# Kernel optimization log

Hardware: AMD Instinct MI355X
Metric: run time of the kernel (lower is better)

Reference implementation:

```python
import jax, jax.numpy as jnp
import numpy as np

B, D = 8192, 1024
GATE_BIAS = 0.0
LN_EPS = 1e-5


def _layernorm(x, w, b):
    mu = jnp.mean(x, axis=-1, keepdims=True)
    var = jnp.mean(jnp.square(x - mu), axis=-1, keepdims=True)
    return (x - mu) * jax.lax.rsqrt(var + LN_EPS) * w + b


def setup_inputs() -> dict:
    key = jax.random.key(0)
    ks = jax.random.split(key, 12)
    s_in = 1.0 / np.sqrt(2 * D)  # torch Linear init scale (fan_in = 2*dim)
    return {
        "x": jax.random.normal(ks[0], (B, D), jnp.float32),
        "h": jax.random.normal(ks[1], (B, D), jnp.float32),
        "ln_w": jnp.ones((2 * D,), jnp.float32),
        "ln_b": jnp.zeros((2 * D,), jnp.float32),
        "ln2_w": jnp.ones((2 * D,), jnp.float32),
        "ln2_b": jnp.zeros((2 * D,), jnp.float32),
        "Wg": jax.random.uniform(ks[2], (5 * D, 2 * D), jnp.float32, -s_in, s_in),
        "bg": jax.random.uniform(ks[3], (5 * D,), jnp.float32, -s_in, s_in),
        "Wu": jax.random.uniform(ks[4], (D, 2 * D), jnp.float32, -s_in, s_in),
        "bu": jax.random.uniform(ks[5], (D,), jnp.float32, -s_in, s_in),
    }


def reference(x, h, ln_w, ln_b, ln2_w, ln2_b, Wg, bg, Wu, bu):
    # eval mode: dropout / dropout_mask (ones) / zoneout are identity
    inp = jnp.concatenate([x, h], axis=1)          # [B, 2D]
    inp = _layernorm(inp, ln_w, ln_b)
    gates = inp @ Wg.T + bg                        # [B, 5D]
    g0, g1, g2, g3, g4 = jnp.split(gates, 5, axis=1)
    rx = jax.nn.sigmoid(g0)
    rh = jax.nn.sigmoid(g1)
    z = jax.nn.softmax(jnp.stack([g2, g3, g4 - GATE_BIAS], axis=-1), axis=-1)  # [B, D, 3]
    inp2 = jnp.concatenate([x * rx, h * rh], axis=1)
    inp2 = _layernorm(inp2, ln2_w, ln2_b)
    u = jnp.tanh(inp2 @ Wu.T + bu)                 # [B, D]
    h_new = (jnp.stack([x, h, u], axis=-1) * z).sum(-1)
    return h_new
```

## Files before the change

### kernel.cpp

```cpp
#include <hip/hip_runtime.h>

typedef __attribute__((ext_vector_type(8))) __bf16 bf16x8;
typedef __attribute__((ext_vector_type(4))) float f32x4;

#define B_ROWS 8192
#define D_DIM  1024
#define K_DIM  2048
#define NG     5120

typedef const __attribute__((address_space(1))) void cg_void;
typedef __attribute__((address_space(3))) void lds_void;

__device__ __forceinline__ float bf2f(unsigned short u) {
    union { unsigned int ui; float f; } c; c.ui = ((unsigned int)u) << 16; return c.f;
}
__device__ __forceinline__ unsigned short f2bf(float f) {
    unsigned int u = __float_as_uint(f);
    unsigned int r = u + 0x7fffu + ((u >> 16) & 1u);
    return (unsigned short)(r >> 16);
}
__device__ __forceinline__ float sigm(float v) { return 1.0f / (1.0f + __expf(-v)); }

__global__ __launch_bounds__(256) void cvt2_f32_bf16(const float* __restrict__ wg,
                                                     const float* __restrict__ wu,
                                                     unsigned short* __restrict__ og,
                                                     unsigned short* __restrict__ ou) {
    const int NG4 = 5120 * 2048 / 4;
    const int NU4 = 1024 * 2048 / 4;
    int i = blockIdx.x * 256 + threadIdx.x;
    if (i < NG4) {
        float4 v = reinterpret_cast<const float4*>(wg)[i];
        ushort4 o; o.x = f2bf(v.x); o.y = f2bf(v.y); o.z = f2bf(v.z); o.w = f2bf(v.w);
        reinterpret_cast<ushort4*>(og)[i] = o;
    } else if (i < NG4 + NU4) {
        int j = i - NG4;
        float4 v = reinterpret_cast<const float4*>(wu)[j];
        ushort4 o; o.x = f2bf(v.x); o.y = f2bf(v.y); o.z = f2bf(v.z); o.w = f2bf(v.w);
        reinterpret_cast<ushort4*>(ou)[j] = o;
    }
}

__global__ __launch_bounds__(256) void ln1_kernel(const float* __restrict__ x, const float* __restrict__ h,
                                                  const float* __restrict__ w, const float* __restrict__ b,
                                                  unsigned short* __restrict__ out) {
    const int row = blockIdx.x;
    const int t = threadIdx.x;
    const float4 xv = reinterpret_cast<const float4*>(x + (size_t)row * D_DIM)[t];
    const float4 hv = reinterpret_cast<const float4*>(h + (size_t)row * D_DIM)[t];
    float s  = xv.x + xv.y + xv.z + xv.w + hv.x + hv.y + hv.z + hv.w;
    float s2 = xv.x*xv.x + xv.y*xv.y + xv.z*xv.z + xv.w*xv.w
             + hv.x*hv.x + hv.y*hv.y + hv.z*hv.z + hv.w*hv.w;
#pragma unroll
    for (int off = 32; off > 0; off >>= 1) { s += __shfl_xor(s, off); s2 += __shfl_xor(s2, off); }
    __shared__ float red[8];
    const int wid = t >> 6, lane = t & 63;
    if (lane == 0) { red[wid] = s; red[4 + wid] = s2; }
    __syncthreads();
    s  = red[0] + red[1] + red[2] + red[3];
    s2 = red[4] + red[5] + red[6] + red[7];
    const float mu  = s * (1.0f / K_DIM);
    const float var = s2 * (1.0f / K_DIM) - mu * mu;
    const float inv = rsqrtf(var + 1e-5f);
    const float4 w0 = reinterpret_cast<const float4*>(w)[t];
    const float4 b0 = reinterpret_cast<const float4*>(b)[t];
    const float4 w1 = reinterpret_cast<const float4*>(w + D_DIM)[t];
    const float4 b1 = reinterpret_cast<const float4*>(b + D_DIM)[t];
    ushort4 o0, o1;
    o0.x = f2bf((xv.x - mu) * inv * w0.x + b0.x);
    o0.y = f2bf((xv.y - mu) * inv * w0.y + b0.y);
    o0.z = f2bf((xv.z - mu) * inv * w0.z + b0.z);
    o0.w = f2bf((xv.w - mu) * inv * w0.w + b0.w);
    o1.x = f2bf((hv.x - mu) * inv * w1.x + b1.x);
    o1.y = f2bf((hv.y - mu) * inv * w1.y + b1.y);
    o1.z = f2bf((hv.z - mu) * inv * w1.z + b1.z);
    o1.w = f2bf((hv.w - mu) * inv * w1.w + b1.w);
    reinterpret_cast<ushort4*>(out + (size_t)row * K_DIM)[t] = o0;
    reinterpret_cast<ushort4*>(out + (size_t)row * K_DIM + D_DIM)[t] = o1;
}

__global__ __launch_bounds__(256) void gate_ln2_kernel(const float* __restrict__ x, const float* __restrict__ h,
                                                       const unsigned short* __restrict__ gates,
                                                       const float* __restrict__ w, const float* __restrict__ b,
                                                       unsigned short* __restrict__ out) {
    const int row = blockIdx.x;
    const int t = threadIdx.x;
    const float4 xv = reinterpret_cast<const float4*>(x + (size_t)row * D_DIM)[t];
    const float4 hv = reinterpret_cast<const float4*>(h + (size_t)row * D_DIM)[t];
    const ushort4 g0v = reinterpret_cast<const ushort4*>(gates + (size_t)row * NG)[t];
    const ushort4 g1v = reinterpret_cast<const ushort4*>(gates + (size_t)row * NG + D_DIM)[t];
    float a0 = xv.x * sigm(bf2f(g0v.x));
    float a1 = xv.y * sigm(bf2f(g0v.y));
    float a2 = xv.z * sigm(bf2f(g0v.z));
    float a3 = xv.w * sigm(bf2f(g0v.w));
    float c0 = hv.x * sigm(bf2f(g1v.x));
    float c1 = hv.y * sigm(bf2f(g1v.y));
    float c2 = hv.z * sigm(bf2f(g1v.z));
    float c3 = hv.w * sigm(bf2f(g1v.w));
    float s  = a0 + a1 + a2 + a3 + c0 + c1 + c2 + c3;
    float s2 = a0*a0 + a1*a1 + a2*a2 + a3*a3 + c0*c0 + c1*c1 + c2*c2 + c3*c3;
#pragma unroll
    for (int off = 32; off > 0; off >>= 1) { s += __shfl_xor(s, off); s2 += __shfl_xor(s2, off); }
    __shared__ float red[8];
    const int wid = t >> 6, lane = t & 63;
    if (lane == 0) { red[wid] = s; red[4 + wid] = s2; }
    __syncthreads();
    s  = red[0] + red[1] + red[2] + red[3];
    s2 = red[4] + red[5] + red[6] + red[7];
    const float mu  = s * (1.0f / K_DIM);
    const float var = s2 * (1.0f / K_DIM) - mu * mu;
    const float inv = rsqrtf(var + 1e-5f);
    const float4 w0 = reinterpret_cast<const float4*>(w)[t];
    const float4 b0 = reinterpret_cast<const float4*>(b)[t];
    const float4 w1 = reinterpret_cast<const float4*>(w + D_DIM)[t];
    const float4 b1 = reinterpret_cast<const float4*>(b + D_DIM)[t];
    ushort4 o0, o1;
    o0.x = f2bf((a0 - mu) * inv * w0.x + b0.x);
    o0.y = f2bf((a1 - mu) * inv * w0.y + b0.y);
    o0.z = f2bf((a2 - mu) * inv * w0.z + b0.z);
    o0.w = f2bf((a3 - mu) * inv * w0.w + b0.w);
    o1.x = f2bf((c0 - mu) * inv * w1.x + b1.x);
    o1.y = f2bf((c1 - mu) * inv * w1.y + b1.y);
    o1.z = f2bf((c2 - mu) * inv * w1.z + b1.z);
    o1.w = f2bf((c3 - mu) * inv * w1.w + b1.w);
    reinterpret_cast<ushort4*>(out + (size_t)row * K_DIM)[t] = o0;
    reinterpret_cast<ushort4*>(out + (size_t)row * K_DIM + D_DIM)[t] = o1;
}

#define PH(BUF, H, KQ, LOADB, STAGE_CODE, VMCNT_CODE) do {                                            \
    bf16x8 aF[4];                                                                                     \
    _Pragma("unroll")                                                                                 \
    for (int m = 0; m < 4; ++m)                                                                       \
        aF[m] = *reinterpret_cast<const bf16x8*>(                                                     \
            &smem[((BUF) * 2 + (H)) * 8192 + ((aRdS[m] ^ ((KQ) * 64)) >> 1)]);                        \
    if (LOADB) {                                                                                      \
        _Pragma("unroll")                                                                             \
        for (int n = 0; n < 4; ++n)                                                                   \
            bF[KQ][n] = *reinterpret_cast<const bf16x8*>(                                             \
                &smem[32768 + ((BUF) * 2 + bHalf) * 8192 + ((bRdS[n] ^ ((KQ) * 64)) >> 1)]);          \
    }                                                                                                 \
    STAGE_CODE;                                                                                       \
    VMCNT_CODE;                                                                                       \
    asm volatile("" ::: "memory");                                                                    \
    __builtin_amdgcn_s_barrier();                                                                     \
    asm volatile("" ::: "memory");                                                                    \
    __builtin_amdgcn_s_setprio(1);                                                                    \
    _Pragma("unroll")                                                                                 \
    for (int m = 0; m < 4; ++m)                                                                       \
        _Pragma("unroll")                                                                             \
        for (int n = 0; n < 4; ++n)                                                                   \
            acc[(H) * 4 + m][n] =                                                                     \
                __builtin_amdgcn_mfma_f32_16x16x32_bf16(aF[m], bF[KQ][n], acc[(H) * 4 + m][n], 0, 0, 0);\
    __builtin_amdgcn_s_setprio(0);                                                                    \
    asm volatile("" ::: "memory");                                                                    \
    __builtin_amdgcn_s_barrier();                                                                     \
    asm volatile("" ::: "memory");                                                                    \
} while (0)

#define VMC4 asm volatile("s_waitcnt vmcnt(4)" ::: "memory")
#define VMC0 asm volatile("s_waitcnt vmcnt(0)" ::: "memory")
#define NOVM (void)0

__global__ __launch_bounds__(512, 2) void gemm_gates8(const unsigned short* __restrict__ A,
                                                      const unsigned short* __restrict__ W,
                                                      const float* __restrict__ bias,
                                                      unsigned short* __restrict__ C) {
    constexpr int K = K_DIM;
    constexpr int NT = K / 64;
    constexpr int NI = NT / 2;
    extern __shared__ unsigned short smem[];

    const int tid = threadIdx.x;
    const int bid = blockIdx.x;
    const int lane = tid & 63;
    const int wid = tid >> 6;
    const int wr = wid >> 2;
    const int wc = wid & 3;
    const int fr = lane & 15;
    const int kb = lane >> 4;
    const int bHalf = wc >> 1;
    const int swzl = (fr & 7) << 4;

    int aRdS[4], bRdS[4];
#pragma unroll
    for (int m = 0; m < 4; ++m)
        aRdS[m] = (((wr * 64 + m * 16 + fr) * 128) + kb * 16) ^ swzl;
#pragma unroll
    for (int n = 0; n < 4; ++n)
        bRdS[n] = ((((wc & 1) * 64 + n * 16 + fr) * 128) + kb * 16) ^ swzl;

    int srcRow[2], srcCol[2], ldsDst[2];
#pragma unroll
    for (int l = 0; l < 2; ++l) {
        const int off = (l * 512 + tid) * 16;
        const int r = off >> 7;
        const int offS = off ^ ((r & 7) << 4);
        srcRow[l] = r;
        srcCol[l] = (offS & 127) >> 1;
        ldsDst[l] = (l * 512 + tid) * 8;
    }

    const int nrep = (bid < 128) ? 2 : 1;
    for (int rep = 0; rep < nrep; ++rep) {
        const int tile = bid + rep * 512;
        const int swz = (tile & 7) * 80 + (tile >> 3);
        const int tm = swz / 20;
        const int tn = swz % 20;
        const int Arow0 = tm * 256;
        const int Brow0 = tn * 256;

        size_t aSrc[2], bSrc[2];
#pragma unroll
        for (int l = 0; l < 2; ++l) {
            aSrc[l] = (size_t)(Arow0 + srcRow[l]) * K + srcCol[l];
            bSrc[l] = (size_t)(Brow0 + srcRow[l]) * K + srcCol[l];
        }

        auto stageA = [&](int buf, int half, int kt) {
#pragma unroll
            for (int l = 0; l < 2; ++l)
                __builtin_amdgcn_global_load_lds(
                    (cg_void*)(A + aSrc[l] + (size_t)half * 128 * K + kt * 64),
                    (lds_void*)(&smem[(buf * 2 + half) * 8192 + ldsDst[l]]), 16, 0, 0);
        };
        auto stageB = [&](int buf, int half, int kt) {
#pragma unroll
            for (int l = 0; l < 2; ++l)
                __builtin_amdgcn_global_load_lds(
                    (cg_void*)(W + bSrc[l] + (size_t)half * 128 * K + kt * 64),
                    (lds_void*)(&smem[32768 + (buf * 2 + half) * 8192 + ldsDst[l]]), 16, 0, 0);
        };

        f32x4 acc[8][4] = {};

        stageA(0, 0, 0); stageA(0, 1, 0); stageB(0, 0, 0); stageB(0, 1, 0);
        stageB(1, 0, 1); stageB(1, 1, 1);
        VMC4;
        asm volatile("" ::: "memory");
        __builtin_amdgcn_s_barrier();
        asm volatile("" ::: "memory");

        for (int i = 0; i < NI; ++i) {
            const int t1 = 2 * i + 1;
            const int t2 = (2 * i + 2) & (NT - 1);
            const int t3 = (2 * i + 3) & (NT - 1);
            bf16x8 bF[2][4];
            PH(0, 0, 0, 1, { stageA(1, 0, t1); stageA(1, 1, t1); }, NOVM);
            PH(0, 0, 1, 1, ;, NOVM);
            PH(0, 1, 0, 0, { stageA(0, 0, t2); }, NOVM);
            PH(0, 1, 1, 0, { stageB(0, 0, t2); }, VMC4);
            PH(1, 0, 0, 1, { stageA(0, 1, t2); stageB(0, 1, t2); }, NOVM);
            PH(1, 0, 1, 1, ;, NOVM);
            PH(1, 1, 0, 0, { stageB(1, 0, t3); }, NOVM);
            PH(1, 1, 1, 0, { stageB(1, 1, t3); }, VMC4);
        }

        VMC0;
        asm volatile("" ::: "memory");
        __builtin_amdgcn_s_barrier();
        asm volatile("" ::: "memory");

        const int crowBase = Arow0 + wr * 64;
        const int ccol = Brow0 + wc * 64;
#pragma unroll
        for (int n = 0; n < 4; ++n) {
            const int c = ccol + n * 16 + fr;
            const float bvv = bias[c];
#pragma unroll
            for (int hh = 0; hh < 2; ++hh)
#pragma unroll
                for (int m = 0; m < 4; ++m) {
                    const size_t r0 = (size_t)crowBase + hh * 128 + m * 16 + kb * 4;
#pragma unroll
                    for (int j = 0; j < 4; ++j)
                        C[(r0 + j) * NG + c] = f2bf(acc[hh * 4 + m][n][j] + bvv);
                }
        }
    }
}

__global__ __launch_bounds__(256) void gemm_out(const unsigned short* __restrict__ A,
                                                const unsigned short* __restrict__ W,
                                                const float* __restrict__ bias,
                                                const unsigned short* __restrict__ gates,
                                                const float* __restrict__ x, const float* __restrict__ h,
                                                float* __restrict__ out) {
    constexpr int K = K_DIM, N = D_DIM;
    __shared__ __attribute__((aligned(16))) unsigned short As[2][128 * 32];
    __shared__ __attribute__((aligned(16))) unsigned short Bs[2][128 * 32];
    const int tid = threadIdx.x;
    const int bid = blockIdx.x;
    const int swz = (bid & 7) * 64 + (bid >> 3);
    const int tn = swz & 7;
    const int tm = swz >> 3;
    const size_t arow0 = (size_t)tm * 128;
    const size_t brow0 = (size_t)tn * 128;

    const int lane = tid & 63;
    const int wid = tid >> 6;
    const int wr = wid >> 1, wc = wid & 1;
    const int fr = lane & 15;
    const int kb = lane >> 4;
    const int aoff = (wr * 64 + fr) * 32 + kb * 8;
    const int boff = (wc * 64 + fr) * 32 + kb * 8;

    f32x4 acc[4][4] = {};

    auto stage = [&](int buf, int k0) {
#pragma unroll
        for (int r = 0; r < 2; ++r) {
            const int idx = r * 256 + tid;
            __builtin_amdgcn_global_load_lds(
                (cg_void*)(A + (arow0 + (idx >> 2)) * K + k0 + (idx & 3) * 8),
                (lds_void*)(&As[buf][idx * 8]), 16, 0, 0);
        }
#pragma unroll
        for (int r = 0; r < 2; ++r) {
            const int idx = r * 256 + tid;
            __builtin_amdgcn_global_load_lds(
                (cg_void*)(W + (brow0 + (idx >> 2)) * K + k0 + (idx & 3) * 8),
                (lds_void*)(&Bs[buf][idx * 8]), 16, 0, 0);
        }
    };

    stage(0, 0);
    __syncthreads();
    int cur = 0;
    constexpr int NT = K / 32;
    for (int t = 0; t < NT; ++t) {
        if (t + 1 < NT) stage(cur ^ 1, (t + 1) * 32);
        bf16x8 af[4], bv[4];
#pragma unroll
        for (int m = 0; m < 4; ++m) af[m] = *reinterpret_cast<const bf16x8*>(&As[cur][aoff + m * 512]);
#pragma unroll
        for (int n = 0; n < 4; ++n) bv[n] = *reinterpret_cast<const bf16x8*>(&Bs[cur][boff + n * 512]);
#pragma unroll
        for (int m = 0; m < 4; ++m)
#pragma unroll
            for (int n = 0; n < 4; ++n)
                acc[m][n] = __builtin_amdgcn_mfma_f32_16x16x32_bf16(af[m], bv[n], acc[m][n], 0, 0, 0);
        __syncthreads();
        cur ^= 1;
    }

    const size_t crow0 = arow0 + wr * 64;
    const int ccol0 = (int)brow0 + wc * 64;
#pragma unroll
    for (int n = 0; n < 4; ++n) {
        const int c = ccol0 + n * 16 + fr;
        const float bvv = bias[c];
#pragma unroll
        for (int m = 0; m < 4; ++m) {
            const size_t r0 = crow0 + m * 16 + kb * 4;
#pragma unroll
            for (int j = 0; j < 4; ++j) {
                const size_t r = r0 + j;
                const float u = tanhf(acc[m][n][j] + bvv);
                const size_t gb = r * NG + c;
                const float g2 = bf2f(gates[gb + 2 * D_DIM]);
                const float g3 = bf2f(gates[gb + 3 * D_DIM]);
                const float g4 = bf2f(gates[gb + 4 * D_DIM]);
                const float mx = fmaxf(fmaxf(g2, g3), g4);
                const float e2 = __expf(g2 - mx), e3 = __expf(g3 - mx), e4 = __expf(g4 - mx);
                const float zi = 1.0f / (e2 + e3 + e4);
                const size_t xi = r * D_DIM + c;
                out[xi] = (x[xi] * e2 + h[xi] * e3 + u * e4) * zi;
            }
        }
    }
}

extern "C" void kernel_launch(void* const* d_in, const int* in_sizes, int n_in,
                              void* d_out, int out_size, void* d_ws, size_t ws_size,
                              hipStream_t stream) {
    const float* x    = (const float*)d_in[0];
    const float* h    = (const float*)d_in[1];
    const float* ln_w = (const float*)d_in[2];
    const float* ln_b = (const float*)d_in[3];
    const float* ln2_w= (const float*)d_in[4];
    const float* ln2_b= (const float*)d_in[5];
    const float* Wg   = (const float*)d_in[6];
    const float* bg   = (const float*)d_in[7];
    const float* Wu   = (const float*)d_in[8];
    const float* bu   = (const float*)d_in[9];
    float* out = (float*)d_out;

    char* ws = (char*)d_ws;
    unsigned short* inp   = (unsigned short*)(ws);
    unsigned short* Wg_b  = (unsigned short*)(ws + 33554432);
    unsigned short* Wu_b  = (unsigned short*)(ws + 33554432 + 20971520);
    unsigned short* gates = (unsigned short*)(ws + 33554432 + 20971520 + 4194304);

    (void)hipFuncSetAttribute((const void*)gemm_gates8,
                              hipFuncAttributeMaxDynamicSharedMemorySize, 131072);

    const int nCvt4 = 5120 * 2048 / 4 + 1024 * 2048 / 4;
    cvt2_f32_bf16<<<(nCvt4 + 255) / 256, 256, 0, stream>>>(Wg, Wu, Wg_b, Wu_b);
    ln1_kernel<<<8192, 256, 0, stream>>>(x, h, ln_w, ln_b, inp);
    gemm_gates8<<<512, 512, 131072, stream>>>(inp, Wg_b, bg, gates);
    gate_ln2_kernel<<<8192, 256, 0, stream>>>(x, h, gates, ln2_w, ln2_b, inp);
    gemm_out<<<512, 256, 0, stream>>>(inp, Wu_b, bu, gates, x, h, out);
}
```

Baseline: 329.0 us.

## Launch one tile per block for gates GEMM and triple-buffer swizzled output GEMM

The gates GEMM now launches 640 blocks, one 256x256 tile each, instead of 512 blocks where the first 128 process two tiles sequentially. This removes the tail where a few blocks do double work. The output GEMM is rewritten to use a three-slot LDS ring with a two-tile prefetch distance, an XOR-swizzled LDS layout to reduce bank conflicts, vmcnt-based waits and setprio around the MFMAs. It also asks for three blocks per CU. The trailing vmcnt(0) drain is dropped, so outstanding wrap-around prefetches may still be in flight when the kernel exits, which is harmless but slightly unusual.

Result: faster. 320.0 us (-2.7%).

```diff
diff --git a/kernel.cpp b/kernel.cpp
--- a/kernel.cpp
+++ b/kernel.cpp
@@ -157,7 +157,6 @@
 } while (0)
 
 #define VMC4 asm volatile("s_waitcnt vmcnt(4)" ::: "memory")
-#define VMC0 asm volatile("s_waitcnt vmcnt(0)" ::: "memory")
 #define NOVM (void)0
 
 __global__ __launch_bounds__(512, 2) void gemm_gates8(const unsigned short* __restrict__ A,
@@ -171,6 +170,12 @@
 
     const int tid = threadIdx.x;
     const int bid = blockIdx.x;
+    const int swz = (bid & 7) * 80 + (bid >> 3);
+    const int tm = swz / 20;
+    const int tn = swz % 20;
+    const int Arow0 = tm * 256;
+    const int Brow0 = tn * 256;
+
     const int lane = tid & 63;
     const int wid = tid >> 6;
     const int wr = wid >> 2;
@@ -188,169 +193,187 @@
     for (int n = 0; n < 4; ++n)
         bRdS[n] = ((((wc & 1) * 64 + n * 16 + fr) * 128) + kb * 16) ^ swzl;
 
-    int srcRow[2], srcCol[2], ldsDst[2];
+    size_t aSrc[2], bSrc[2];
+    int ldsDst[2];
 #pragma unroll
     for (int l = 0; l < 2; ++l) {
         const int off = (l * 512 + tid) * 16;
         const int r = off >> 7;
         const int offS = off ^ ((r & 7) << 4);
-        srcRow[l] = r;
-        srcCol[l] = (offS & 127) >> 1;
+        const int cb = (offS & 127) >> 1;
+        aSrc[l] = (size_t)(Arow0 + r) * K + cb;
+        bSrc[l] = (size_t)(Brow0 + r) * K + cb;
         ldsDst[l] = (l * 512 + tid) * 8;
     }
 
-    const int nrep = (bid < 128) ? 2 : 1;
-    for (int rep = 0; rep < nrep; ++rep) {
-        const int tile = bid + rep * 512;
-        const int swz = (tile & 7) * 80 + (tile >> 3);
-        const int tm = swz / 20;
-        const int tn = swz % 20;
-        const int Arow0 = tm * 256;
-        const int Brow0 = tn * 256;
-
-        size_t aSrc[2], bSrc[2];
-#pragma unroll
-        for (int l = 0; l < 2; ++l) {
-            aSrc[l] = (size_t)(Arow0 + srcRow[l]) * K + srcCol[l];
-            bSrc[l] = (size_t)(Brow0 + srcRow[l]) * K + srcCol[l];
-        }
-
-        auto stageA = [&](int buf, int half, int kt) {
-#pragma unroll
-            for (int l = 0; l < 2; ++l)
-                __builtin_amdgcn_global_load_lds(
-                    (cg_void*)(A + aSrc[l] + (size_t)half * 128 * K + kt * 64),
-                    (lds_void*)(&smem[(buf * 2 + half) * 8192 + ldsDst[l]]), 16, 0, 0);
-        };
-        auto stageB = [&](int buf, int half, int kt) {
-#pragma unroll
-            for (int l = 0; l < 2; ++l)
-                __builtin_amdgcn_global_load_lds(
-                    (cg_void*)(W + bSrc[l] + (size_t)half * 128 * K + kt * 64),
-                    (lds_void*)(&smem[32768 + (buf * 2 + half) * 8192 + ldsDst[l]]), 16, 0, 0);
-        };
-
-        f32x4 acc[8][4] = {};
-
-        stageA(0, 0, 0); stageA(0, 1, 0); stageB(0, 0, 0); stageB(0, 1, 0);
-        stageB(1, 0, 1); stageB(1, 1, 1);
-        VMC4;
-        asm volatile("" ::: "memory");
-        __builtin_amdgcn_s_barrier();
-        asm volatile("" ::: "memory");
-
-        for (int i = 0; i < NI; ++i) {
-            const int t1 = 2 * i + 1;
-            const int t2 = (2 * i + 2) & (NT - 1);
-            const int t3 = (2 * i + 3) & (NT - 1);
-            bf16x8 bF[2][4];
-            PH(0, 0, 0, 1, { stageA(1, 0, t1); stageA(1, 1, t1); }, NOVM);
-            PH(0, 0, 1, 1, ;, NOVM);
-            PH(0, 1, 0, 0, { stageA(0, 0, t2); }, NOVM);
-            PH(0, 1, 1, 0, { stageB(0, 0, t2); }, VMC4);
-            PH(1, 0, 0, 1, { stageA(0, 1, t2); stageB(0, 1, t2); }, NOVM);
-            PH(1, 0, 1, 1, ;, NOVM);
-            PH(1, 1, 0, 0, { stageB(1, 0, t3); }, NOVM);
-            PH(1, 1, 1, 0, { stageB(1, 1, t3); }, VMC4);
-        }
-
-        VMC0;
-        asm volatile("" ::: "memory");
-        __builtin_amdgcn_s_barrier();
-        asm volatile("" ::: "memory");
-
-        const int crowBase = Arow0 + wr * 64;
-        const int ccol = Brow0 + wc * 64;
-#pragma unroll
-        for (int n = 0; n < 4; ++n) {
-            const int c = ccol + n * 16 + fr;
-            const float bvv = bias[c];
-#pragma unroll
-            for (int hh = 0; hh < 2; ++hh)
-#pragma unroll
-                for (int m = 0; m < 4; ++m) {
-                    const size_t r0 = (size_t)crowBase + hh * 128 + m * 16 + kb * 4;
-#pragma unroll
-                    for (int j = 0; j < 4; ++j)
-                        C[(r0 + j) * NG + c] = f2bf(acc[hh * 4 + m][n][j] + bvv);
-                }
-        }
-    }
-}
-
-__global__ __launch_bounds__(256) void gemm_out(const unsigned short* __restrict__ A,
-                                                const unsigned short* __restrict__ W,
-                                                const float* __restrict__ bias,
-                                                const unsigned short* __restrict__ gates,
-                                                const float* __restrict__ x, const float* __restrict__ h,
-                                                float* __restrict__ out) {
-    constexpr int K = K_DIM, N = D_DIM;
-    __shared__ __attribute__((aligned(16))) unsigned short As[2][128 * 32];
-    __shared__ __attribute__((aligned(16))) unsigned short Bs[2][128 * 32];
+    auto stageA = [&](int buf, int half, int kt) {
+#pragma unroll
+        for (int l = 0; l < 2; ++l)
+            __builtin_amdgcn_global_load_lds(
+                (cg_void*)(A + aSrc[l] + (size_t)half * 128 * K + kt * 64),
+                (lds_void*)(&smem[(buf * 2 + half) * 8192 + ldsDst[l]]), 16, 0, 0);
+    };
+    auto stageB = [&](int buf, int half, int kt) {
+#pragma unroll
+        for (int l = 0; l < 2; ++l)
+            __builtin_amdgcn_global_load_lds(
+                (cg_void*)(W + bSrc[l] + (size_t)half * 128 * K + kt * 64),
+                (lds_void*)(&smem[32768 + (buf * 2 + half) * 8192 + ldsDst[l]]), 16, 0, 0);
+    };
+
+    f32x4 acc[8][4] = {};
+
+    stageA(0, 0, 0); stageA(0, 1, 0); stageB(0, 0, 0); stageB(0, 1, 0);
+    stageB(1, 0, 1); stageB(1, 1, 1);
+    VMC4;
+    asm volatile("" ::: "memory");
+    __builtin_amdgcn_s_barrier();
+    asm volatile("" ::: "memory");
+
+    for (int i = 0; i < NI; ++i) {
+        const int t1 = 2 * i + 1;
+        const int t2 = (2 * i + 2) & (NT - 1);
+        const int t3 = (2 * i + 3) & (NT - 1);
+        bf16x8 bF[2][4];
+        PH(0, 0, 0, 1, { stageA(1, 0, t1); stageA(1, 1, t1); }, NOVM);
+        PH(0, 0, 1, 1, ;, NOVM);
+        PH(0, 1, 0, 0, { stageA(0, 0, t2); }, NOVM);
+        PH(0, 1, 1, 0, { stageB(0, 0, t2); }, VMC4);
+        PH(1, 0, 0, 1, { stageA(0, 1, t2); stageB(0, 1, t2); }, NOVM);
+        PH(1, 0, 1, 1, ;, NOVM);
+        PH(1, 1, 0, 0, { stageB(1, 0, t3); }, NOVM);
+        PH(1, 1, 1, 0, { stageB(1, 1, t3); }, VMC4);
+    }
+
+    const int crowBase = Arow0 + wr * 64;
+    const int ccol = Brow0 + wc * 64;
+#pragma unroll
+    for (int n = 0; n < 4; ++n) {
+        const int c = ccol + n * 16 + fr;
+        const float bvv = bias[c];
+#pragma unroll
+        for (int hh = 0; hh < 2; ++hh)
+#pragma unroll
+            for (int m = 0; m < 4; ++m) {
+                const size_t r0 = (size_t)crowBase + hh * 128 + m * 16 + kb * 4;
+#pragma unroll
+                for (int j = 0; j < 4; ++j)
+                    C[(r0 + j) * NG + c] = f2bf(acc[hh * 4 + m][n][j] + bvv);
+            }
+    }
+}
+
+__global__ __launch_bounds__(256, 3) void gemm_out3(const unsigned short* __restrict__ A,
+                                                    const unsigned short* __restrict__ W,
+                                                    const float* __restrict__ bias,
+                                                    const unsigned short* __restrict__ gates,
+                                                    const float* __restrict__ x, const float* __restrict__ h,
+                                                    float* __restrict__ out) {
+    constexpr int K = K_DIM;
+    constexpr int NTK = K / 32;
+    extern __shared__ unsigned short smem[];
+
     const int tid = threadIdx.x;
     const int bid = blockIdx.x;
     const int swz = (bid & 7) * 64 + (bid >> 3);
     const int tn = swz & 7;
     const int tm = swz >> 3;
-    const size_t arow0 = (size_t)tm * 128;
-    const size_t brow0 = (size_t)tn * 128;
+    const int Arow0 = tm * 128;
+    const int Brow0 = tn * 128;
 
     const int lane = tid & 63;
     const int wid = tid >> 6;
-    const int wr = wid >> 1, wc = wid & 1;
+    const int wr = wid >> 1;
+    const int wc = wid & 1;
     const int fr = lane & 15;
     const int kb = lane >> 4;
-    const int aoff = (wr * 64 + fr) * 32 + kb * 8;
-    const int boff = (wc * 64 + fr) * 32 + kb * 8;
+
+    int aRd[4], bRd[4];
+#pragma unroll
+    for (int m = 0; m < 4; ++m) {
+        const int row = wr * 64 + m * 16 + fr;
+        aRd[m] = ((row >> 1) * 128 + ((((row & 1) * 64) + kb * 16) ^ (((row >> 1) & 7) << 4))) >> 1;
+    }
+#pragma unroll
+    for (int n = 0; n < 4; ++n) {
+        const int row = wc * 64 + n * 16 + fr;
+        bRd[n] = ((row >> 1) * 128 + ((((row & 1) * 64) + kb * 16) ^ (((row >> 1) & 7) << 4))) >> 1;
+    }
+
+    size_t aSrcB[2], bSrcB[2];
+#pragma unroll
+    for (int l = 0; l < 2; ++l) {
+        const int t2 = l * 256 + tid;
+        const int line = t2 >> 3;
+        const int inB = (t2 & 7) * 16;
+        const int inBS = inB ^ ((line & 7) << 4);
+        const int row = line * 2 + (inBS >> 6);
+        const int col = (inBS & 63) >> 1;
+        aSrcB[l] = (size_t)(Arow0 + row) * K + col;
+        bSrcB[l] = (size_t)(Brow0 + row) * K + col;
+    }
+
+    auto stage = [&](int slot, int kt) {
+#pragma unroll
+        for (int l = 0; l < 2; ++l)
+            __builtin_amdgcn_global_load_lds((cg_void*)(A + aSrcB[l] + kt * 32),
+                                             (lds_void*)(&smem[slot * 4096 + (l * 256 + tid) * 8]), 16, 0, 0);
+#pragma unroll
+        for (int l = 0; l < 2; ++l)
+            __builtin_amdgcn_global_load_lds((cg_void*)(W + bSrcB[l] + kt * 32),
+                                             (lds_void*)(&smem[12288 + slot * 4096 + (l * 256 + tid) * 8]), 16, 0, 0);
+    };
 
     f32x4 acc[4][4] = {};
 
-    auto stage = [&](int buf, int k0) {
-#pragma unroll
-        for (int r = 0; r < 2; ++r) {
-            const int idx = r * 256 + tid;
-            __builtin_amdgcn_global_load_lds(
-                (cg_void*)(A + (arow0 + (idx >> 2)) * K + k0 + (idx & 3) * 8),
-                (lds_void*)(&As[buf][idx * 8]), 16, 0, 0);
-        }
-#pragma unroll
-        for (int r = 0; r < 2; ++r) {
-            const int idx = r * 256 + tid;
-            __builtin_amdgcn_global_load_lds(
-                (cg_void*)(W + (brow0 + (idx >> 2)) * K + k0 + (idx & 3) * 8),
-                (lds_void*)(&Bs[buf][idx * 8]), 16, 0, 0);
-        }
-    };
-
-    stage(0, 0);
-    __syncthreads();
-    int cur = 0;
-    constexpr int NT = K / 32;
-    for (int t = 0; t < NT; ++t) {
-        if (t + 1 < NT) stage(cur ^ 1, (t + 1) * 32);
-        bf16x8 af[4], bv[4];
-#pragma unroll
-        for (int m = 0; m < 4; ++m) af[m] = *reinterpret_cast<const bf16x8*>(&As[cur][aoff + m * 512]);
-#pragma unroll
-        for (int n = 0; n < 4; ++n) bv[n] = *reinterpret_cast<const bf16x8*>(&Bs[cur][boff + n * 512]);
+    stage(0, 0); stage(1, 1);
+    VMC4;
+    asm volatile("" ::: "memory");
+    __builtin_amdgcn_s_barrier();
+    asm volatile("" ::: "memory");
+
+    int sC = 0;
+    for (int t = 0; t < NTK; ++t) {
+        const int sP = (sC == 0) ? 2 : sC - 1;
+        const int kt2 = (t + 2) & (NTK - 1);
+
+        bf16x8 aF[4], bF[4];
 #pragma unroll
         for (int m = 0; m < 4; ++m)
+            aF[m] = *reinterpret_cast<const bf16x8*>(&smem[sC * 4096 + aRd[m]]);
+#pragma unroll
+        for (int n = 0; n < 4; ++n)
+            bF[n] = *reinterpret_cast<const bf16x8*>(&smem[12288 + sC * 4096 + bRd[n]]);
+
+        stage(sP, kt2);
+        VMC4;
+        asm volatile("" ::: "memory");
+        __builtin_amdgcn_s_barrier();
+        asm volatile("" ::: "memory");
+
+        __builtin_amdgcn_s_setprio(1);
+#pragma unroll
+        for (int m = 0; m < 4; ++m)
 #pragma unroll
             for (int n = 0; n < 4; ++n)
-                acc[m][n] = __builtin_amdgcn_mfma_f32_16x16x32_bf16(af[m], bv[n], acc[m][n], 0, 0, 0);
-        __syncthreads();
-        cur ^= 1;
-    }
-
-    const size_t crow0 = arow0 + wr * 64;
-    const int ccol0 = (int)brow0 + wc * 64;
+                acc[m][n] = __builtin_amdgcn_mfma_f32_16x16x32_bf16(aF[m], bF[n], acc[m][n], 0, 0, 0);
+        __builtin_amdgcn_s_setprio(0);
+        asm volatile("" ::: "memory");
+        __builtin_amdgcn_s_barrier();
+        asm volatile("" ::: "memory");
+
+        sC = (sC == 2) ? 0 : sC + 1;
+    }
+
+    const int crow0 = Arow0 + wr * 64;
+    const int ccol0 = Brow0 + wc * 64;
 #pragma unroll
     for (int n = 0; n < 4; ++n) {
         const int c = ccol0 + n * 16 + fr;
         const float bvv = bias[c];
 #pragma unroll
         for (int m = 0; m < 4; ++m) {
-            const size_t r0 = crow0 + m * 16 + kb * 4;
+            const size_t r0 = (size_t)crow0 + m * 16 + kb * 4;
 #pragma unroll
             for (int j = 0; j < 4; ++j) {
                 const size_t r = r0 + j;
@@ -392,11 +415,13 @@
 
     (void)hipFuncSetAttribute((const void*)gemm_gates8,
                               hipFuncAttributeMaxDynamicSharedMemorySize, 131072);
+    (void)hipFuncSetAttribute((const void*)gemm_out3,
+                              hipFuncAttributeMaxDynamicSharedMemorySize, 49152);
 
     const int nCvt4 = 5120 * 2048 / 4 + 1024 * 2048 / 4;
     cvt2_f32_bf16<<<(nCvt4 + 255) / 256, 256, 0, stream>>>(Wg, Wu, Wg_b, Wu_b);
     ln1_kernel<<<8192, 256, 0, stream>>>(x, h, ln_w, ln_b, inp);
-    gemm_gates8<<<512, 512, 131072, stream>>>(inp, Wg_b, bg, gates);
+    gemm_gates8<<<640, 512, 131072, stream>>>(inp, Wg_b, bg, gates);
     gate_ln2_kernel<<<8192, 256, 0, stream>>>(x, h, gates, ln2_w, ln2_b, inp);
-    gemm_out<<<512, 256, 0, stream>>>(inp, Wu_b, bu, gates, x, h, out);
-}
+    gemm_out3<<<512, 256, 49152, stream>>>(inp, Wu_b, bu, gates, x, h, out);
+}
```
